# Optimization experiments

Hardware: AMD Instinct MI355X
Metric: run time of the kernel (lower is better)

## Reference

```python
import jax, jax.numpy as jnp
import numpy as np

N_NODES = 200000
N_EDGES = 3200000
VOCAB = 10000
D = 25
EPS = 1e-5


def setup_inputs() -> dict:
    key = jax.random.key(0)
    ks = jax.random.split(key, 16)
    x = jax.random.randint(ks[0], (N_NODES,), 0, VOCAB)
    edge_index = jax.random.randint(ks[1], (2, N_EDGES), 0, N_NODES)
    s = 1.0 / np.sqrt(D)
    inp = {
        'x': x,
        'edge_index': edge_index,
        'emb': jax.random.normal(ks[2], (VOCAB, D), jnp.float32),
        'W1': jax.random.normal(ks[3], (D, D), jnp.float32) * s,
        'b1': jnp.zeros((D,), jnp.float32),
        'g1': jnp.ones((D,), jnp.float32),
        'be1': jnp.zeros((D,), jnp.float32),
        'W2': jax.random.normal(ks[4], (D, D), jnp.float32) * s,
        'b2': jnp.zeros((D,), jnp.float32),
        'g2': jnp.ones((D,), jnp.float32),
        'be2': jnp.zeros((D,), jnp.float32),
        'Wm1': jax.random.normal(ks[5], (D, 12), jnp.float32) * s,
        'bm1': jnp.zeros((12,), jnp.float32),
        'Wm2': jax.random.normal(ks[6], (12, 1), jnp.float32) * (1.0 / np.sqrt(12)),
        'bm2': jnp.zeros((1,), jnp.float32),
    }
    return inp


def gcn_conv(h, src, dst, W, b):
    # PyG GCNConv: h @ W, symmetric normalization with self-loops, scatter-add, + bias
    n = h.shape[0]
    h = h @ W
    loops = jnp.arange(n)
    s = jnp.concatenate([src, loops])  # sources j
    d = jnp.concatenate([dst, loops])  # targets i
    deg = jax.ops.segment_sum(jnp.ones_like(d, h.dtype), d, num_segments=n)
    dinv = jnp.where(deg > 0, jax.lax.rsqrt(jnp.maximum(deg, 1.0)), 0.0)
    norm = dinv[s] * dinv[d]  # [E+N]
    msg = h[s] * norm[:, None]
    out = jax.ops.segment_sum(msg, d, num_segments=n)
    return out + b


def batch_norm(h, g, b):
    mu = jnp.mean(h, axis=0)
    var = jnp.mean((h - mu) ** 2, axis=0)
    return (h - mu) * jax.lax.rsqrt(var + EPS) * g + b


def reference(x, edge_index, emb, W1, b1, g1, be1, W2, b2, g2, be2, Wm1, bm1, Wm2, bm2):
    src, dst = edge_index[0], edge_index[1]
    h = emb[x]  # [N, 25]
    h = jax.nn.relu(batch_norm(gcn_conv(h, src, dst, W1, b1), g1, be1))
    h = jax.nn.relu(batch_norm(gcn_conv(h, src, dst, W2, b2), g2, be2))
    h = jax.nn.relu(h @ Wm1 + bm1)
    return jax.nn.sigmoid(h @ Wm2 + bm2)  # [N, 1]
```

## Files before the change

kernel.cpp:

```cpp
#include <hip/hip_runtime.h>
#include <hip/hip_fp16.h>
#include <math.h>

#define D 25
#define PH_STRIDE 32
#define STATS_BLOCKS 512
#define NBK 256
#define BIN_EDGES 8192
#define NSLOT 64
#define EPS 1e-5f

__global__ __launch_bounds__(256) void binA(const int* __restrict__ dst,
                                            int* __restrict__ hist2D, int E) {
    __shared__ int h[NBK];
    h[threadIdx.x] = 0;
    __syncthreads();
    int base = blockIdx.x * BIN_EDGES;
#pragma unroll
    for (int j = 0; j < 32; ++j) {
        int idx = base + j * 256 + threadIdx.x;
        if (idx < E) atomicAdd(&h[dst[idx] >> 10], 1);
    }
    __syncthreads();
    hist2D[blockIdx.x * NBK + threadIdx.x] = h[threadIdx.x];
}

__global__ __launch_bounds__(512) void colscan(int* __restrict__ hist2D,
                                               int* __restrict__ bCount, int nbBin) {
    __shared__ int s[512];
    int b = blockIdx.x;
    int j = threadIdx.x;
    int v = (j < nbBin) ? hist2D[j * NBK + b] : 0;
    s[j] = v;
    __syncthreads();
    for (int off = 1; off < 512; off <<= 1) {
        int x = (j >= off) ? s[j - off] : 0;
        __syncthreads();
        s[j] += x;
        __syncthreads();
    }
    if (j < nbBin) hist2D[j * NBK + b] = s[j] - v;
    if (j == 0) bCount[b] = s[511];
}

__global__ __launch_bounds__(256) void binB(const int* __restrict__ src,
                                            const int* __restrict__ dst,
                                            const int* __restrict__ hist2D,
                                            const int* __restrict__ bCount,
                                            int* __restrict__ binned, int E) {
    __shared__ int rank[NBK], basew[NBK], sc[NBK];
    int t = threadIdx.x;
    int cnt = bCount[t];
    sc[t] = cnt;
    rank[t] = 0;
    __syncthreads();
    for (int off = 1; off < NBK; off <<= 1) {
        int x = (t >= off) ? sc[t - off] : 0;
        __syncthreads();
        sc[t] += x;
        __syncthreads();
    }
    basew[t] = (sc[t] - cnt) + hist2D[blockIdx.x * NBK + t];
    __syncthreads();
    int base = blockIdx.x * BIN_EDGES;
#pragma unroll
    for (int j = 0; j < 32; ++j) {
        int idx = base + j * 256 + t;
        if (idx < E) {
            int d = dst[idx];
            int b = d >> 10;
            int r = atomicAdd(&rank[b], 1);
            binned[basew[b] + r] = (src[idx] << 10) | (d & 1023);
        }
    }
}

__global__ __launch_bounds__(512) void bucket_fill(const int* __restrict__ binned,
                                                   const int* __restrict__ bCount,
                                                   int* __restrict__ degi, int* __restrict__ cursor,
                                                   int* __restrict__ csr, int N) {
    int b = blockIdx.x;
    int nodeBase = b << 10;
    if (nodeBase >= N) return;
    __shared__ int h[1024];
    __shared__ int s2[512];
    int t = threadIdx.x;
    if (t < 256) s2[t] = (t < b) ? bCount[t] : 0;
    __syncthreads();
    for (int off = 128; off > 0; off >>= 1) {
        if (t < off) s2[t] += s2[t + off];
        __syncthreads();
    }
    int s = s2[0];
    __syncthreads();
    h[t] = 0; h[t + 512] = 0;
    __syncthreads();
    int e = s + bCount[b];
    for (int k = s + t; k < e; k += 512)
        atomicAdd(&h[binned[k] & 1023], 1);
    __syncthreads();
    int i0 = t * 2;
    int v0 = h[i0], v1 = h[i0 + 1];
    int node0 = nodeBase + i0;
    if (node0 < N) degi[node0] = v0;
    if (node0 + 1 < N) degi[node0 + 1] = v1;
    s2[t] = v0 + v1;
    __syncthreads();
    for (int off = 1; off < 512; off <<= 1) {
        int x = (t >= off) ? s2[t - off] : 0;
        __syncthreads();
        s2[t] += x;
        __syncthreads();
    }
    int pre = (t > 0) ? s2[t - 1] : 0;
    h[i0] = pre;
    h[i0 + 1] = pre + v0;
    __syncthreads();
    for (int k = s + t; k < e; k += 512) {
        int key = binned[k];
        int p = atomicAdd(&h[key & 1023], 1);
        csr[s + p] = key >> 10;
    }
    __syncthreads();
    if (node0 < N) cursor[node0] = s + h[i0];
    if (node0 + 1 < N) cursor[node0 + 1] = s + h[i0 + 1];
}

__global__ void hist_kernel(const int* __restrict__ dst, int* __restrict__ degi, int E) {
    int e = blockIdx.x * blockDim.x + threadIdx.x;
    if (e < E) atomicAdd(&degi[dst[e]], 1);
}

__global__ __launch_bounds__(256) void embed_gemm1_h(
        const int* __restrict__ x, const float* __restrict__ emb,
        const float* __restrict__ W1, const int* __restrict__ degi,
        __half* __restrict__ Ph, int N) {
    __shared__ float sW[D * D];
    for (int j = threadIdx.x; j < D * D; j += blockDim.x) sW[j] = W1[j];
    __syncthreads();
    int i = blockIdx.x * blockDim.x + threadIdx.x;
    if (i >= N) return;
    const float* er = emb + (size_t)x[i] * D;
    float t[D];
#pragma unroll
    for (int k = 0; k < D; ++k) t[k] = er[k];
    float dinv = rsqrtf((float)degi[i] + 1.0f);
    __half* row = Ph + (size_t)i * PH_STRIDE;
#pragma unroll
    for (int d = 0; d < D; ++d) {
        float acc = 0.0f;
#pragma unroll
        for (int k = 0; k < D; ++k) acc = fmaf(t[k], sW[k * D + d], acc);
        row[d] = __float2half(dinv * acc);
    }
#pragma unroll
    for (int d = D; d < PH_STRIDE; ++d) row[d] = __float2half(0.0f);
}

__global__ __launch_bounds__(256) void gather_stats_w8(
        const int* __restrict__ csr, const int* __restrict__ cursor,
        const int* __restrict__ degi, const __half* __restrict__ Ph,
        const float* __restrict__ bias, float* __restrict__ Q,
        float* __restrict__ stPart, int N) {
    int t = threadIdx.x;
    int node = blockIdx.x * 16 + (t >> 4);
    int f = t & 15;
    const __half2* rowb = (const __half2*)Ph;
    float q0 = 0.0f, q1 = 0.0f;
    bool act = (node < N);
    if (act) {
        int end = cursor[node];
        int dg = degi[node];
        int k = end - dg;
        float2 sv = __half22float2(rowb[((size_t)node << 4) + f]);
        float ax = sv.x, ay = sv.y;
        for (; k + 8 <= end; k += 8) {
            int s0 = csr[k],     s1 = csr[k + 1], s2 = csr[k + 2], s3 = csr[k + 3];
            int s4 = csr[k + 4], s5 = csr[k + 5], s6 = csr[k + 6], s7 = csr[k + 7];
            float2 v0 = __half22float2(rowb[((size_t)s0 << 4) + f]);
            float2 v1 = __half22float2(rowb[((size_t)s1 << 4) + f]);
            float2 v2 = __half22float2(rowb[((size_t)s2 << 4) + f]);
            float2 v3 = __half22float2(rowb[((size_t)s3 << 4) + f]);
            float2 v4 = __half22float2(rowb[((size_t)s4 << 4) + f]);
            float2 v5 = __half22float2(rowb[((size_t)s5 << 4) + f]);
            float2 v6 = __half22float2(rowb[((size_t)s6 << 4) + f]);
            float2 v7 = __half22float2(rowb[((size_t)s7 << 4) + f]);
            ax += ((v0.x + v1.x) + (v2.x + v3.x)) + ((v4.x + v5.x) + (v6.x + v7.x));
            ay += ((v0.y + v1.y) + (v2.y + v3.y)) + ((v4.y + v5.y) + (v6.y + v7.y));
        }
        for (; k + 4 <= end; k += 4) {
            int s0 = csr[k], s1 = csr[k + 1], s2 = csr[k + 2], s3 = csr[k + 3];
            float2 v0 = __half22float2(rowb[((size_t)s0 << 4) + f]);
            float2 v1 = __half22float2(rowb[((size_t)s1 << 4) + f]);
            float2 v2 = __half22float2(rowb[((size_t)s2 << 4) + f]);
            float2 v3 = __half22float2(rowb[((size_t)s3 << 4) + f]);
            ax += (v0.x + v1.x) + (v2.x + v3.x);
            ay += (v0.y + v1.y) + (v2.y + v3.y);
        }
        for (; k < end; ++k) {
            float2 v = __half22float2(rowb[((size_t)csr[k] << 4) + f]);
            ax += v.x; ay += v.y;
        }
        float dinv = rsqrtf((float)dg + 1.0f);
        if (f < 13) {
            int j0 = f << 1;
            q0 = fmaf(dinv, ax, bias[j0]);
            Q[(size_t)node * D + j0] = q0;
            if (f < 12) {
                q1 = fmaf(dinv, ay, bias[j0 + 1]);
                Q[(size_t)node * D + j0 + 1] = q1;
            }
        }
    }
    float ls0 = q0, lq0 = q0 * q0, ls1 = q1, lq1 = q1 * q1;
    ls0 += __shfl_down(ls0, 32, 64); ls0 += __shfl_down(ls0, 16, 64);
    lq0 += __shfl_down(lq0, 32, 64); lq0 += __shfl_down(lq0, 16, 64);
    ls1 += __shfl_down(ls1, 32, 64); ls1 += __shfl_down(ls1, 16, 64);
    lq1 += __shfl_down(lq1, 32, 64); lq1 += __shfl_down(lq1, 16, 64);
    __shared__ float red[4][16][4];
    if ((t & 63) < 16) {
        int w = t >> 6;
        red[w][f][0] = ls0; red[w][f][1] = lq0;
        red[w][f][2] = ls1; red[w][f][3] = lq1;
    }
    __syncthreads();
    if (t < 64) {
        int ff = t >> 2, slot = t & 3;
        float tot = red[0][ff][slot] + red[1][ff][slot] + red[2][ff][slot] + red[3][ff][slot];
        int a = 2 * ff + (slot >> 1);
        if (a < D) atomicAdd(&stPart[(blockIdx.x & (NSLOT - 1)) * 50 + a + (slot & 1) * D], tot);
    }
}

__global__ __launch_bounds__(256) void bn_gemm_hp(
        const float* __restrict__ Qin, const float* __restrict__ stPart, float invN,
        const float* __restrict__ g, const float* __restrict__ be,
        const float* __restrict__ W, const int* __restrict__ degi,
        __half* __restrict__ Ph, int N) {
    __shared__ float sW[D * D];
    __shared__ float sScale[D], sShift[D];
    __shared__ float sSum[2 * D];
    for (int j = threadIdx.x; j < D * D; j += blockDim.x) sW[j] = W[j];
    if (threadIdx.x < 2 * D) {
        float a = 0.0f;
        for (int k = 0; k < NSLOT; ++k) a += stPart[k * 50 + threadIdx.x];
        sSum[threadIdx.x] = a;
    }
    __syncthreads();
    if (threadIdx.x < D) {
        float m = sSum[threadIdx.x] * invN;
        float v = fmaxf(sSum[D + threadIdx.x] * invN - m * m, 0.0f);
        float sc = rsqrtf(v + EPS) * g[threadIdx.x];
        sScale[threadIdx.x] = sc;
        sShift[threadIdx.x] = be[threadIdx.x] - m * sc;
    }
    __syncthreads();
    int i = blockIdx.x * blockDim.x + threadIdx.x;
    if (i >= N) return;
    float t[D];
#pragma unroll
    for (int d = 0; d < D; ++d)
        t[d] = fmaxf(0.0f, fmaf(Qin[i * D + d], sScale[d], sShift[d]));
    float dinv = rsqrtf((float)degi[i] + 1.0f);
    __half* row = Ph + (size_t)i * PH_STRIDE;
#pragma unroll
    for (int d = 0; d < D; ++d) {
        float acc = 0.0f;
#pragma unroll
        for (int k = 0; k < D; ++k) acc = fmaf(t[k], sW[k * D + d], acc);
        row[d] = __float2half(dinv * acc);
    }
#pragma unroll
    for (int d = D; d < PH_STRIDE; ++d) row[d] = __float2half(0.0f);
}

__global__ __launch_bounds__(256) void final_kernel_p(
        const float* __restrict__ Q, const float* __restrict__ stPart, float invN,
        const float* __restrict__ g, const float* __restrict__ be,
        const float* __restrict__ Wm1, const float* __restrict__ bm1,
        const float* __restrict__ Wm2, const float* __restrict__ bm2,
        float* __restrict__ out, int N) {
    __shared__ float sW1[D * 12];
    __shared__ float sb1[12], sW2[12];
    __shared__ float sScale[D], sShift[D];
    __shared__ float sSum[2 * D];
    __shared__ float sb2;
    for (int j = threadIdx.x; j < D * 12; j += blockDim.x) sW1[j] = Wm1[j];
    if (threadIdx.x < 12) {
        sb1[threadIdx.x] = bm1[threadIdx.x];
        sW2[threadIdx.x] = Wm2[threadIdx.x];
    }
    if (threadIdx.x < 2 * D) {
        float a = 0.0f;
        for (int k = 0; k < NSLOT; ++k) a += stPart[k * 50 + threadIdx.x];
        sSum[threadIdx.x] = a;
    }
    if (threadIdx.x == 0) sb2 = bm2[0];
    __syncthreads();
    if (threadIdx.x < D) {
        float m = sSum[threadIdx.x] * invN;
        float v = fmaxf(sSum[D + threadIdx.x] * invN - m * m, 0.0f);
        float sc = rsqrtf(v + EPS) * g[threadIdx.x];
        sScale[threadIdx.x] = sc;
        sShift[threadIdx.x] = be[threadIdx.x] - m * sc;
    }
    __syncthreads();
    int i = blockIdx.x * blockDim.x + threadIdx.x;
    if (i >= N) return;
    float t[D];
#pragma unroll
    for (int d = 0; d < D; ++d)
        t[d] = fmaxf(0.0f, fmaf(Q[i * D + d], sScale[d], sShift[d]));
    float z = sb2;
#pragma unroll
    for (int j = 0; j < 12; ++j) {
        float m = sb1[j];
#pragma unroll
        for (int k = 0; k < D; ++k) m = fmaf(t[k], sW1[k * 12 + j], m);
        m = fmaxf(0.0f, m);
        z = fmaf(m, sW2[j], z);
    }
    out[i] = 1.0f / (1.0f + expf(-z));
}

__global__ __launch_bounds__(256) void embed_gemm1(
        const int* __restrict__ x, const float* __restrict__ emb,
        const float* __restrict__ W1, const int* __restrict__ degi,
        float* __restrict__ P, float* __restrict__ Qdup, int N) {
    __shared__ float sW[D * D];
    for (int j = threadIdx.x; j < D * D; j += blockDim.x) sW[j] = W1[j];
    __syncthreads();
    int i = blockIdx.x * blockDim.x + threadIdx.x;
    if (i >= N) return;
    const float* er = emb + (size_t)x[i] * D;
    float t[D];
#pragma unroll
    for (int k = 0; k < D; ++k) t[k] = er[k];
    float dinv = rsqrtf((float)degi[i] + 1.0f);
#pragma unroll
    for (int d = 0; d < D; ++d) {
        float acc = 0.0f;
#pragma unroll
        for (int k = 0; k < D; ++k) acc = fmaf(t[k], sW[k * D + d], acc);
        float v = dinv * acc;
        P[i * D + d] = v;
        if (Qdup) Qdup[i * D + d] = v;
    }
}

__global__ void scatter_kernel(const int* __restrict__ src, const int* __restrict__ dst,
                               const float* __restrict__ A, float* __restrict__ B, int E) {
    int idx = blockIdx.x * blockDim.x + threadIdx.x;
    int e = idx >> 5;
    int lane = idx & 31;
    if (e >= E || lane >= D) return;
    atomicAdd(&B[dst[e] * D + lane], A[src[e] * D + lane]);
}

__global__ __launch_bounds__(256) void transform_kernel(
        float* __restrict__ Q, const int* __restrict__ degi,
        const float* __restrict__ bias, int N) {
    int i = blockIdx.x * blockDim.x + threadIdx.x;
    if (i >= N) return;
    float dinv = rsqrtf((float)degi[i] + 1.0f);
#pragma unroll
    for (int d = 0; d < D; ++d)
        Q[i * D + d] = fmaf(dinv, Q[i * D + d], bias[d]);
}

__global__ __launch_bounds__(256) void stats_kernel(
        const float* __restrict__ Q, float* __restrict__ st, int N) {
    float ls[D], lq[D];
#pragma unroll
    for (int d = 0; d < D; ++d) { ls[d] = 0.0f; lq[d] = 0.0f; }
    for (int i = blockIdx.x * blockDim.x + threadIdx.x; i < N;
         i += gridDim.x * blockDim.x) {
#pragma unroll
        for (int d = 0; d < D; ++d) {
            float v = Q[i * D + d];
            ls[d] += v;
            lq[d] += v * v;
        }
    }
#pragma unroll
    for (int d = 0; d < D; ++d) {
        for (int off = 32; off > 0; off >>= 1) {
            ls[d] += __shfl_down(ls[d], off, 64);
            lq[d] += __shfl_down(lq[d], off, 64);
        }
    }
    __shared__ float red[4][2 * D];
    int wave = threadIdx.x >> 6;
    int lane = threadIdx.x & 63;
    if (lane == 0) {
#pragma unroll
        for (int d = 0; d < D; ++d) {
            red[wave][d] = ls[d];
            red[wave][D + d] = lq[d];
        }
    }
    __syncthreads();
    if (threadIdx.x < 2 * D) {
        float t = red[0][threadIdx.x] + red[1][threadIdx.x] +
                  red[2][threadIdx.x] + red[3][threadIdx.x];
        atomicAdd(&st[threadIdx.x], t);
    }
}

__global__ __launch_bounds__(256) void bn_gemm(
        const float* __restrict__ Qin, const float* __restrict__ st, float invN,
        const float* __restrict__ g, const float* __restrict__ be,
        const float* __restrict__ W, const int* __restrict__ degi,
        float* __restrict__ P, float* __restrict__ Qdup, int N) {
    __shared__ float sW[D * D];
    __shared__ float sScale[D], sShift[D];
    for (int j = threadIdx.x; j < D * D; j += blockDim.x) sW[j] = W[j];
    if (threadIdx.x < D) {
        float m = st[threadIdx.x] * invN;
        float v = fmaxf(st[D + threadIdx.x] * invN - m * m, 0.0f);
        float sc = rsqrtf(v + EPS) * g[threadIdx.x];
        sScale[threadIdx.x] = sc;
        sShift[threadIdx.x] = be[threadIdx.x] - m * sc;
    }
    __syncthreads();
    int i = blockIdx.x * blockDim.x + threadIdx.x;
    if (i >= N) return;
    float t[D];
#pragma unroll
    for (int d = 0; d < D; ++d)
        t[d] = fmaxf(0.0f, fmaf(Qin[i * D + d], sScale[d], sShift[d]));
    float dinv = rsqrtf((float)degi[i] + 1.0f);
#pragma unroll
    for (int d = 0; d < D; ++d) {
        float acc = 0.0f;
#pragma unroll
        for (int k = 0; k < D; ++k) acc = fmaf(t[k], sW[k * D + d], acc);
        float v = dinv * acc;
        P[i * D + d] = v;
        if (Qdup) Qdup[i * D + d] = v;
    }
}

__global__ __launch_bounds__(256) void final_kernel(
        const float* __restrict__ Q, const float* __restrict__ st, float invN,
        const float* __restrict__ g, const float* __restrict__ be,
        const float* __restrict__ Wm1, const float* __restrict__ bm1,
        const float* __restrict__ Wm2, const float* __restrict__ bm2,
        float* __restrict__ out, int N) {
    __shared__ float sW1[D * 12];
    __shared__ float sb1[12], sW2[12];
    __shared__ float sScale[D], sShift[D];
    __shared__ float sb2;
    for (int j = threadIdx.x; j < D * 12; j += blockDim.x) sW1[j] = Wm1[j];
    if (threadIdx.x < 12) {
        sb1[threadIdx.x] = bm1[threadIdx.x];
        sW2[threadIdx.x] = Wm2[threadIdx.x];
    }
    if (threadIdx.x < D) {
        float m = st[threadIdx.x] * invN;
        float v = fmaxf(st[D + threadIdx.x] * invN - m * m, 0.0f);
        float sc = rsqrtf(v + EPS) * g[threadIdx.x];
        sScale[threadIdx.x] = sc;
        sShift[threadIdx.x] = be[threadIdx.x] - m * sc;
    }
    if (threadIdx.x == 0) sb2 = bm2[0];
    __syncthreads();
    int i = blockIdx.x * blockDim.x + threadIdx.x;
    if (i >= N) return;
    float t[D];
#pragma unroll
    for (int d = 0; d < D; ++d)
        t[d] = fmaxf(0.0f, fmaf(Q[i * D + d], sScale[d], sShift[d]));
    float z = sb2;
#pragma unroll
    for (int j = 0; j < 12; ++j) {
        float m = sb1[j];
#pragma unroll
        for (int k = 0; k < D; ++k) m = fmaf(t[k], sW1[k * 12 + j], m);
        m = fmaxf(0.0f, m);
        z = fmaf(m, sW2[j], z);
    }
    out[i] = 1.0f / (1.0f + expf(-z));
}

extern "C" void kernel_launch(void* const* d_in, const int* in_sizes, int n_in,
                              void* d_out, int out_size, void* d_ws, size_t ws_size,
                              hipStream_t stream) {
    const int*   x    = (const int*)d_in[0];
    const int*   ei   = (const int*)d_in[1];
    const float* emb  = (const float*)d_in[2];
    const float* W1   = (const float*)d_in[3];
    const float* b1   = (const float*)d_in[4];
    const float* g1   = (const float*)d_in[5];
    const float* be1  = (const float*)d_in[6];
    const float* W2   = (const float*)d_in[7];
    const float* b2   = (const float*)d_in[8];
    const float* g2   = (const float*)d_in[9];
    const float* be2  = (const float*)d_in[10];
    const float* Wm1  = (const float*)d_in[11];
    const float* bm1  = (const float*)d_in[12];
    const float* Wm2  = (const float*)d_in[13];
    const float* bm2  = (const float*)d_in[14];
    float* out = (float*)d_out;

    int N = in_sizes[0];
    int E = in_sizes[1] / 2;
    const int* src = ei;
    const int* dst = ei + E;
    float invN = 1.0f / (float)N;

    int nbBin = (E + BIN_EDGES - 1) / BIN_EDGES;
    size_t csrNeed = ((size_t)43 * N + E + 256 + (size_t)nbBin * NBK + 2 * NSLOT * 50) * 4;
    bool useCSR = (ws_size >= csrNeed) && (N <= NBK * 1024) && (nbBin <= 512) &&
                  ((size_t)E <= (size_t)N * D);

    int nbN  = (N + 255) / 256;
    int nbE  = (E + 255) / 256;
    int nbG  = (N + 15) / 16;
    int nbS  = (int)(((long)E * 32 + 255) / 256);

    if (useCSR) {
        int*    degi    = (int*)d_ws;
        int*    cursor  = degi + N;
        int*    csr     = cursor + N;
        int*    bCount  = csr + E;
        int*    hist2D  = bCount + NBK;
        __half* Ph      = (__half*)(hist2D + (size_t)nbBin * NBK);
        float*  Q       = (float*)(Ph + (size_t)N * PH_STRIDE);
        float*  stP1    = Q + (size_t)N * D;
        float*  stP2    = stP1 + NSLOT * 50;
        int*    binned  = (int*)Q;

        hipMemsetAsync(stP1, 0, 2 * NSLOT * 50 * sizeof(float), stream);

        int nbBkt = (N + 1023) / 1024;

        binA<<<nbBin, 256, 0, stream>>>(dst, hist2D, E);
        colscan<<<NBK, 512, 0, stream>>>(hist2D, bCount, nbBin);
        binB<<<nbBin, 256, 0, stream>>>(src, dst, hist2D, bCount, binned, E);
        bucket_fill<<<nbBkt, 512, 0, stream>>>(binned, bCount, degi, cursor, csr, N);
        embed_gemm1_h<<<nbN, 256, 0, stream>>>(x, emb, W1, degi, Ph, N);
        gather_stats_w8<<<nbG, 256, 0, stream>>>(csr, cursor, degi, Ph, b1, Q, stP1, N);
        bn_gemm_hp<<<nbN, 256, 0, stream>>>(Q, stP1, invN, g1, be1, W2, degi, Ph, N);
        gather_stats_w8<<<nbG, 256, 0, stream>>>(csr, cursor, degi, Ph, b2, Q, stP2, N);
        final_kernel_p<<<nbN, 256, 0, stream>>>(Q, stP2, invN, g2, be2, Wm1, bm1, Wm2, bm2, out, N);
    } else {
        int*   degi  = (int*)d_ws;
        float* P     = (float*)(degi + N);
        float* Q     = P + (size_t)N * D;
        float* stats = Q + (size_t)N * D;
        float* st1 = stats;
        float* st2 = stats + 50;

        hipMemsetAsync(degi, 0, (size_t)N * sizeof(int), stream);
        hipMemsetAsync(stats, 0, 100 * sizeof(float), stream);

        hist_kernel<<<nbE, 256, 0, stream>>>(dst, degi, E);
        embed_gemm1<<<nbN, 256, 0, stream>>>(x, emb, W1, degi, P, Q, N);
        scatter_kernel<<<nbS, 256, 0, stream>>>(src, dst, P, Q, E);
        transform_kernel<<<nbN, 256, 0, stream>>>(Q, degi, b1, N);
        stats_kernel<<<STATS_BLOCKS, 256, 0, stream>>>(Q, st1, N);
        bn_gemm<<<nbN, 256, 0, stream>>>(Q, st1, invN, g1, be1, W2, degi, P, Q, N);
        scatter_kernel<<<nbS, 256, 0, stream>>>(src, dst, P, Q, E);
        transform_kernel<<<nbN, 256, 0, stream>>>(Q, degi, b2, N);
        stats_kernel<<<STATS_BLOCKS, 256, 0, stream>>>(Q, st2, N);
        final_kernel<<<nbN, 256, 0, stream>>>(Q, st2, invN, g2, be2, Wm1, bm1, Wm2, bm2, out, N);
    }
}
```

Before: 335.7 us.

## Fuse embedding GEMM into bucket fill, store Q in fp16, drop memset

The first-layer embedding GEMM now runs at the end of the CSR bucket-fill kernel, using the degrees that kernel already computed, which removes one launch and a re-read of degi. The intermediate Q activations are stored as padded fp16 half2 rows instead of fp32, roughly halving their write and read traffic in the gather and BN kernels. The stats-partials memset is folded into binA. In exchange the activations lose precision, and the CSR path now requires at least 25 bin blocks and E <= 16N. Fill blocks use 512 threads each with two nodes per thread doing the GEMM, so GEMM parallelism is lower.

After: 332.4 us. About the same (-1.0%).

```diff
diff --git a/kernel.cpp b/kernel.cpp
--- a/kernel.cpp
+++ b/kernel.cpp
@@ -11,7 +11,9 @@
 #define EPS 1e-5f
 
 __global__ __launch_bounds__(256) void binA(const int* __restrict__ dst,
-                                            int* __restrict__ hist2D, int E) {
+                                            int* __restrict__ hist2D,
+                                            float* __restrict__ stPart, int E) {
+    if (blockIdx.x < 25) stPart[blockIdx.x * 256 + threadIdx.x] = 0.0f;
     __shared__ int h[NBK];
     h[threadIdx.x] = 0;
     __syncthreads();
@@ -75,20 +77,24 @@
     }
 }
 
-__global__ __launch_bounds__(512) void bucket_fill(const int* __restrict__ binned,
-                                                   const int* __restrict__ bCount,
-                                                   int* __restrict__ degi, int* __restrict__ cursor,
-                                                   int* __restrict__ csr, int N) {
+__global__ __launch_bounds__(512) void fill_embed(
+        const int* __restrict__ binned, const int* __restrict__ bCount,
+        const int* __restrict__ x, const float* __restrict__ emb,
+        const float* __restrict__ W1,
+        int* __restrict__ degi, int* __restrict__ cursor, int* __restrict__ csr,
+        __half* __restrict__ Ph, int N) {
     int b = blockIdx.x;
     int nodeBase = b << 10;
     if (nodeBase >= N) return;
     __shared__ int h[1024];
     __shared__ int s2[512];
+    __shared__ float sW[D * D];
     int t = threadIdx.x;
     if (t < 256) s2[t] = (t < b) ? bCount[t] : 0;
+    for (int j = t; j < D * D; j += 512) sW[j] = W1[j];
     __syncthreads();
     for (int off = 128; off > 0; off >>= 1) {
-        if (t < off) s2[t] += s2[t + off];
+        if (t < 128 && t < off) s2[t] += s2[t + off];
         __syncthreads();
     }
     int s = s2[0];
@@ -107,9 +113,9 @@
     s2[t] = v0 + v1;
     __syncthreads();
     for (int off = 1; off < 512; off <<= 1) {
-        int x = (t >= off) ? s2[t - off] : 0;
-        __syncthreads();
-        s2[t] += x;
+        int xx = (t >= off) ? s2[t - off] : 0;
+        __syncthreads();
+        s2[t] += xx;
         __syncthreads();
     }
     int pre = (t > 0) ? s2[t - 1] : 0;
@@ -124,51 +130,40 @@
     __syncthreads();
     if (node0 < N) cursor[node0] = s + h[i0];
     if (node0 + 1 < N) cursor[node0 + 1] = s + h[i0 + 1];
-}
-
-__global__ void hist_kernel(const int* __restrict__ dst, int* __restrict__ degi, int E) {
-    int e = blockIdx.x * blockDim.x + threadIdx.x;
-    if (e < E) atomicAdd(&degi[dst[e]], 1);
-}
-
-__global__ __launch_bounds__(256) void embed_gemm1_h(
-        const int* __restrict__ x, const float* __restrict__ emb,
-        const float* __restrict__ W1, const int* __restrict__ degi,
-        __half* __restrict__ Ph, int N) {
-    __shared__ float sW[D * D];
-    for (int j = threadIdx.x; j < D * D; j += blockDim.x) sW[j] = W1[j];
-    __syncthreads();
-    int i = blockIdx.x * blockDim.x + threadIdx.x;
-    if (i >= N) return;
-    const float* er = emb + (size_t)x[i] * D;
-    float t[D];
-#pragma unroll
-    for (int k = 0; k < D; ++k) t[k] = er[k];
-    float dinv = rsqrtf((float)degi[i] + 1.0f);
-    __half* row = Ph + (size_t)i * PH_STRIDE;
-#pragma unroll
-    for (int d = 0; d < D; ++d) {
-        float acc = 0.0f;
-#pragma unroll
-        for (int k = 0; k < D; ++k) acc = fmaf(t[k], sW[k * D + d], acc);
-        row[d] = __float2half(dinv * acc);
-    }
-#pragma unroll
-    for (int d = D; d < PH_STRIDE; ++d) row[d] = __float2half(0.0f);
+#pragma unroll
+    for (int which = 0; which < 2; ++which) {
+        int node = node0 + which;
+        if (node >= N) break;
+        int dg = which ? v1 : v0;
+        const float* er = emb + (size_t)x[node] * D;
+        float tv[D];
+#pragma unroll
+        for (int k = 0; k < D; ++k) tv[k] = er[k];
+        float dinv = rsqrtf((float)dg + 1.0f);
+        __half* row = Ph + (size_t)node * PH_STRIDE;
+#pragma unroll
+        for (int d = 0; d < D; ++d) {
+            float acc = 0.0f;
+#pragma unroll
+            for (int k = 0; k < D; ++k) acc = fmaf(tv[k], sW[k * D + d], acc);
+            row[d] = __float2half(dinv * acc);
+        }
+#pragma unroll
+        for (int d = D; d < PH_STRIDE; ++d) row[d] = __float2half(0.0f);
+    }
 }
 
 __global__ __launch_bounds__(256) void gather_stats_w8(
         const int* __restrict__ csr, const int* __restrict__ cursor,
         const int* __restrict__ degi, const __half* __restrict__ Ph,
-        const float* __restrict__ bias, float* __restrict__ Q,
+        const float* __restrict__ bias, __half* __restrict__ Qh,
         float* __restrict__ stPart, int N) {
     int t = threadIdx.x;
     int node = blockIdx.x * 16 + (t >> 4);
     int f = t & 15;
     const __half2* rowb = (const __half2*)Ph;
     float q0 = 0.0f, q1 = 0.0f;
-    bool act = (node < N);
-    if (act) {
+    if (node < N) {
         int end = cursor[node];
         int dg = degi[node];
         int k = end - dg;
@@ -205,11 +200,8 @@
         if (f < 13) {
             int j0 = f << 1;
             q0 = fmaf(dinv, ax, bias[j0]);
-            Q[(size_t)node * D + j0] = q0;
-            if (f < 12) {
-                q1 = fmaf(dinv, ay, bias[j0 + 1]);
-                Q[(size_t)node * D + j0 + 1] = q1;
-            }
+            if (f < 12) q1 = fmaf(dinv, ay, bias[j0 + 1]);
+            ((__half2*)Qh)[((size_t)node << 4) + f] = __floats2half2_rn(q0, q1);
         }
     }
     float ls0 = q0, lq0 = q0 * q0, ls1 = q1, lq1 = q1 * q1;
@@ -233,7 +225,7 @@
 }
 
 __global__ __launch_bounds__(256) void bn_gemm_hp(
-        const float* __restrict__ Qin, const float* __restrict__ stPart, float invN,
+        const __half* __restrict__ Qh, const float* __restrict__ stPart, float invN,
         const float* __restrict__ g, const float* __restrict__ be,
         const float* __restrict__ W, const int* __restrict__ degi,
         __half* __restrict__ Ph, int N) {
@@ -257,10 +249,15 @@
     __syncthreads();
     int i = blockIdx.x * blockDim.x + threadIdx.x;
     if (i >= N) return;
+    const __half2* qrow = (const __half2*)Qh + ((size_t)i << 4);
     float t[D];
 #pragma unroll
-    for (int d = 0; d < D; ++d)
-        t[d] = fmaxf(0.0f, fmaf(Qin[i * D + d], sScale[d], sShift[d]));
+    for (int ff = 0; ff < 13; ++ff) {
+        float2 v = __half22float2(qrow[ff]);
+        int j0 = ff << 1;
+        t[j0] = fmaxf(0.0f, fmaf(v.x, sScale[j0], sShift[j0]));
+        if (ff < 12) t[j0 + 1] = fmaxf(0.0f, fmaf(v.y, sScale[j0 + 1], sShift[j0 + 1]));
+    }
     float dinv = rsqrtf((float)degi[i] + 1.0f);
     __half* row = Ph + (size_t)i * PH_STRIDE;
 #pragma unroll
@@ -275,7 +272,7 @@
 }
 
 __global__ __launch_bounds__(256) void final_kernel_p(
-        const float* __restrict__ Q, const float* __restrict__ stPart, float invN,
+        const __half* __restrict__ Qh, const float* __restrict__ stPart, float invN,
         const float* __restrict__ g, const float* __restrict__ be,
         const float* __restrict__ Wm1, const float* __restrict__ bm1,
         const float* __restrict__ Wm2, const float* __restrict__ bm2,
@@ -307,10 +304,15 @@
     __syncthreads();
     int i = blockIdx.x * blockDim.x + threadIdx.x;
     if (i >= N) return;
+    const __half2* qrow = (const __half2*)Qh + ((size_t)i << 4);
     float t[D];
 #pragma unroll
-    for (int d = 0; d < D; ++d)
-        t[d] = fmaxf(0.0f, fmaf(Q[i * D + d], sScale[d], sShift[d]));
+    for (int ff = 0; ff < 13; ++ff) {
+        float2 v = __half22float2(qrow[ff]);
+        int j0 = ff << 1;
+        t[j0] = fmaxf(0.0f, fmaf(v.x, sScale[j0], sShift[j0]));
+        if (ff < 12) t[j0 + 1] = fmaxf(0.0f, fmaf(v.y, sScale[j0 + 1], sShift[j0 + 1]));
+    }
     float z = sb2;
 #pragma unroll
     for (int j = 0; j < 12; ++j) {
@@ -321,6 +323,11 @@
         z = fmaf(m, sW2[j], z);
     }
     out[i] = 1.0f / (1.0f + expf(-z));
+}
+
+__global__ void hist_kernel(const int* __restrict__ dst, int* __restrict__ degi, int E) {
+    int e = blockIdx.x * blockDim.x + threadIdx.x;
+    if (e < E) atomicAdd(&degi[dst[e]], 1);
 }
 
 __global__ __launch_bounds__(256) void embed_gemm1(
@@ -510,9 +517,9 @@
     float invN = 1.0f / (float)N;
 
     int nbBin = (E + BIN_EDGES - 1) / BIN_EDGES;
-    size_t csrNeed = ((size_t)43 * N + E + 256 + (size_t)nbBin * NBK + 2 * NSLOT * 50) * 4;
+    size_t csrNeed = ((size_t)34 * N + E + 256 + (size_t)nbBin * NBK + 2 * NSLOT * 50) * 4;
     bool useCSR = (ws_size >= csrNeed) && (N <= NBK * 1024) && (nbBin <= 512) &&
-                  ((size_t)E <= (size_t)N * D);
+                  ((size_t)E <= (size_t)16 * N) && (nbBin >= 25);
 
     int nbN  = (N + 255) / 256;
     int nbE  = (E + 255) / 256;
@@ -526,24 +533,22 @@
         int*    bCount  = csr + E;
         int*    hist2D  = bCount + NBK;
         __half* Ph      = (__half*)(hist2D + (size_t)nbBin * NBK);
-        float*  Q       = (float*)(Ph + (size_t)N * PH_STRIDE);
-        float*  stP1    = Q + (size_t)N * D;
+        __half* Qh      = Ph + (size_t)N * PH_STRIDE;
+        float*  stP1    = (float*)(Qh + (size_t)N * PH_STRIDE);
         float*  stP2    = stP1 + NSLOT * 50;
-        int*    binned  = (int*)Q;
-
-        hipMemsetAsync(stP1, 0, 2 * NSLOT * 50 * sizeof(float), stream);
+        int*    binned  = (int*)Qh;
 
         int nbBkt = (N + 1023) / 1024;
 
-        binA<<<nbBin, 256, 0, stream>>>(dst, hist2D, E);
+        binA<<<nbBin, 256, 0, stream>>>(dst, hist2D, stP1, E);
         colscan<<<NBK, 512, 0, stream>>>(hist2D, bCount, nbBin);
         binB<<<nbBin, 256, 0, stream>>>(src, dst, hist2D, bCount, binned, E);
-        bucket_fill<<<nbBkt, 512, 0, stream>>>(binned, bCount, degi, cursor, csr, N);
-        embed_gemm1_h<<<nbN, 256, 0, stream>>>(x, emb, W1, degi, Ph, N);
-        gather_stats_w8<<<nbG, 256, 0, stream>>>(csr, cursor, degi, Ph, b1, Q, stP1, N);
-        bn_gemm_hp<<<nbN, 256, 0, stream>>>(Q, stP1, invN, g1, be1, W2, degi, Ph, N);
-        gather_stats_w8<<<nbG, 256, 0, stream>>>(csr, cursor, degi, Ph, b2, Q, stP2, N);
-        final_kernel_p<<<nbN, 256, 0, stream>>>(Q, stP2, invN, g2, be2, Wm1, bm1, Wm2, bm2, out, N);
+        fill_embed<<<nbBkt, 512, 0, stream>>>(binned, bCount, x, emb, W1,
+                                              degi, cursor, csr, Ph, N);
+        gather_stats_w8<<<nbG, 256, 0, stream>>>(csr, cursor, degi, Ph, b1, Qh, stP1, N);
+        bn_gemm_hp<<<nbN, 256, 0, stream>>>(Qh, stP1, invN, g1, be1, W2, degi, Ph, N);
+        gather_stats_w8<<<nbG, 256, 0, stream>>>(csr, cursor, degi, Ph, b2, Qh, stP2, N);
+        final_kernel_p<<<nbN, 256, 0, stream>>>(Qh, stP2, invN, g2, be2, Wm1, bm1, Wm2, bm2, out, N);
     } else {
         int*   degi  = (int*)d_ws;
         float* P     = (float*)(degi + N);
```
